# Kernel optimization log

Measured on AMD Instinct MI355X. Metric: run time of the kernel, lower is better.

The kernel has to match this reference:

```python
import jax, jax.numpy as jnp
import numpy as np

N_NODES = 50000
W_IN = 256
W_OUT = 256
HEADS = 8
D_HEAD = W_OUT // HEADS
NUM_EDGE = 3
N_EDGES = 800000
NEG_SLOPE = 0.2


def setup_inputs() -> dict:
    key = jax.random.key(0)
    ks = jax.random.split(key, 10)
    x = jax.random.normal(ks[0], (N_NODES, W_IN), dtype=jnp.float32)
    adj = jax.random.randint(ks[1], (NUM_EDGE, 2, N_EDGES), 0, N_NODES, dtype=jnp.int64)
    sw = 1.0 / np.sqrt(W_IN)
    # Per-edge-type GATConv params, stacked on leading edge-type axis
    Ws = jax.random.normal(ks[2], (NUM_EDGE, W_IN, HEADS * D_HEAD), dtype=jnp.float32) * sw
    a_l = jax.random.normal(ks[3], (NUM_EDGE, HEADS, D_HEAD), dtype=jnp.float32) * 0.1
    a_r = jax.random.normal(ks[4], (NUM_EDGE, HEADS, D_HEAD), dtype=jnp.float32) * 0.1
    bias = jnp.zeros((NUM_EDGE, HEADS * D_HEAD), dtype=jnp.float32)
    # Semantic attention layer: Linear(w_out -> 1)
    att_w = jax.random.normal(ks[5], (W_OUT, 1), dtype=jnp.float32) * (1.0 / np.sqrt(W_OUT))
    att_b = jnp.zeros((1,), dtype=jnp.float32)
    return {"x": x, "adj": adj, "Ws": Ws, "a_l": a_l, "a_r": a_r,
            "bias": bias, "att_w": att_w, "att_b": att_b}


def _gat(x, edge_index, W, al, ar, b):
    # x: [N, W_IN]; edge_index: [2, E]; W: [W_IN, H*D]; al/ar: [H, D]; b: [H*D]
    N = x.shape[0]
    h = (x @ W).reshape(N, HEADS, D_HEAD)            # [N, H, D]
    src, dst = edge_index[0], edge_index[1]
    el = jnp.einsum('nhd,hd->nh', h, al)             # src-side scores [N, H]
    er = jnp.einsum('nhd,hd->nh', h, ar)             # dst-side scores [N, H]
    e = jax.nn.leaky_relu(el[src] + er[dst], NEG_SLOPE)   # [E, H]
    # segment softmax over incoming edges of each dst node
    m = jax.ops.segment_max(e, dst, num_segments=N)       # [N, H]
    e = jnp.exp(e - m[dst])
    s = jax.ops.segment_sum(e, dst, num_segments=N)       # [N, H]
    alpha = e / (s[dst] + 1e-9)                           # [E, H]
    out = jax.ops.segment_sum(alpha[:, :, None] * h[src], dst, num_segments=N)
    return out.reshape(N, HEADS * D_HEAD) + b             # concat heads [N, W_OUT]


def reference(x, adj, Ws, a_l, a_r, bias, att_w, att_b):
    outs = [_gat(x, adj[i], Ws[i], a_l[i], a_r[i], bias[i]) for i in range(NUM_EDGE)]
    stacked = jnp.stack(outs, axis=1)                     # [N, T, W_OUT]
    # AttentionLayer: scores = Linear(stacked) viewed as [N, 1, T]; NO softmax (faithful)
    att = (stacked @ att_w + att_b).reshape(-1, 1, NUM_EDGE)  # [N, 1, T]
    return jnp.matmul(att, stacked).squeeze(1)            # [N, W_OUT]
```

## Files before the change

### kernel.cpp

```cpp
#include <hip/hip_runtime.h>

#define N_NODES 50000
#define W_IN    256
#define W_OUT   256
#define HEADS   8
#define NUM_T   3
#define N_EDGES 800000
#define NEG_SLOPE 0.2f

#define NB      128
#define BSH     9
#define BNODES  512
#define P1_EPT  16
#define P1_CHUNK (256 * P1_EPT)
#define P1_BLOCKS ((N_EDGES + P1_CHUNK - 1) / P1_CHUNK)
#define NB_USED ((N_NODES + BNODES - 1) / BNODES)

typedef __attribute__((ext_vector_type(8))) short bf16x8;
typedef __attribute__((ext_vector_type(4))) float f32x4;

__device__ __forceinline__ unsigned short f2b(float f) {
    unsigned u = __float_as_uint(f);
    u = (u + 0x7fffu + ((u >> 16) & 1u)) >> 16;
    return (unsigned short)u;
}
__device__ __forceinline__ float blo(unsigned u) { return __uint_as_float(u << 16); }
__device__ __forceinline__ float bhi(unsigned u) { return __uint_as_float(u & 0xffff0000u); }

__global__ __launch_bounds__(256) void convert_x(const float* __restrict__ x,
                                                 unsigned short* __restrict__ xb) {
    const size_t i = ((size_t)blockIdx.x * 256 + threadIdx.x) * 4;
    const float4 v = *(const float4*)(x + i);
    ushort4 o;
    o.x = f2b(v.x); o.y = f2b(v.y); o.z = f2b(v.z); o.w = f2b(v.w);
    *(ushort4*)(xb + i) = o;
}

__global__ __launch_bounds__(256) void convert_W(const float* __restrict__ Wsrc,
                                                 unsigned short* __restrict__ Wt) {
    const int t = blockIdx.y;
    const int gid = blockIdx.x * 256 + threadIdx.x;
    const int k = gid >> 8, n = gid & 255;
    Wt[(size_t)t * 65536 + (size_t)n * 256 + k] = f2b(Wsrc[(size_t)t * 65536 + gid]);
}

__global__ __launch_bounds__(256) void p1_hist(const int* __restrict__ adj,
                                               int* __restrict__ bucket_cnt) {
    __shared__ int lh[NB];
    const int t = blockIdx.y;
    const int tid = threadIdx.x;
    if (tid < NB) lh[tid] = 0;
    __syncthreads();

    const int* dstp = adj + (size_t)t * 2 * N_EDGES + N_EDGES;
    const int e0 = blockIdx.x * P1_CHUNK + tid * P1_EPT;
#pragma unroll
    for (int i = 0; i < P1_EPT; ++i) {
        const int e = e0 + i;
        if (e < N_EDGES) atomicAdd(&lh[dstp[e] >> BSH], 1);
    }
    __syncthreads();
    if (tid < NB && lh[tid] > 0) atomicAdd(&bucket_cnt[t * NB + tid], lh[tid]);
}

__global__ __launch_bounds__(128) void p1_scan(const int* __restrict__ bucket_cnt,
                                               int* __restrict__ bucket_ptr,
                                               int* __restrict__ bucket_cur) {
    __shared__ int s[NB];
    const int tid = threadIdx.x;
    for (int t = 0; t < NUM_T; ++t) {
        const int v = bucket_cnt[t * NB + tid];
        s[tid] = v;
        __syncthreads();
        for (int off = 1; off < NB; off <<= 1) {
            int o = (tid >= off) ? s[tid - off] : 0;
            __syncthreads();
            s[tid] += o;
            __syncthreads();
        }
        const int incl = s[tid];
        const int excl = incl - v;
        bucket_ptr[t * (NB + 1) + tid] = excl;
        bucket_cur[t * NB + tid] = excl;
        if (tid == NB - 1) bucket_ptr[t * (NB + 1) + NB] = incl;
        __syncthreads();
    }
}

__global__ __launch_bounds__(256) void p1_scatter(const int* __restrict__ adj,
                                                  int* __restrict__ bucket_cur,
                                                  uint2* __restrict__ part) {
    __shared__ int lh[NB];
    __shared__ int loff[NB];
    __shared__ int lbase[NB];
    __shared__ uint2 buf[P1_CHUNK];
    const int t = blockIdx.y;
    const int tid = threadIdx.x;
    const int lane = tid & 63;
    const int wave = tid >> 6;
    if (tid < NB) lh[tid] = 0;
    __syncthreads();

    const int* srcp = adj + (size_t)t * 2 * N_EDGES;
    const int* dstp = srcp + N_EDGES;
    const int e0 = blockIdx.x * P1_CHUNK + tid * P1_EPT;

    int es[P1_EPT], ed[P1_EPT], rk[P1_EPT];
#pragma unroll
    for (int i = 0; i < P1_EPT; ++i) {
        const int e = e0 + i;
        if (e < N_EDGES) {
            es[i] = srcp[e];
            ed[i] = dstp[e];
            rk[i] = atomicAdd(&lh[ed[i] >> BSH], 1);
        } else {
            ed[i] = -1;
        }
    }
    __syncthreads();

    if (tid < NB && lh[tid] > 0)
        lbase[tid] = atomicAdd(&bucket_cur[t * NB + tid], lh[tid]);
    if (wave == 0) {
        const int c0 = lh[lane * 2], c1 = lh[lane * 2 + 1];
        const int s = c0 + c1;
        int run = s;
        for (int off = 1; off < 64; off <<= 1) {
            const int o = __shfl_up(run, off);
            if (lane >= off) run += o;
        }
        const int base = run - s;
        loff[lane * 2] = base;
        loff[lane * 2 + 1] = base + c0;
    }
    __syncthreads();

#pragma unroll
    for (int i = 0; i < P1_EPT; ++i)
        if (ed[i] >= 0)
            buf[loff[ed[i] >> BSH] + rk[i]] =
                make_uint2((unsigned)es[i], (unsigned)ed[i]);
    __syncthreads();

    uint2* pt = part + (size_t)t * N_EDGES;
    int nvalid = N_EDGES - blockIdx.x * P1_CHUNK;
    if (nvalid > P1_CHUNK) nvalid = P1_CHUNK;
    for (int idx = tid; idx < nvalid; idx += 256) {
        const uint2 e = buf[idx];
        const int b = (int)(e.y >> BSH);
        pt[lbase[b] + (idx - loff[b])] = e;
    }
}

__global__ __launch_bounds__(256) void p2_csr(const uint2* __restrict__ part,
                                              const int* __restrict__ bucket_ptr,
                                              int* __restrict__ row_ptr_all,
                                              int* __restrict__ csr_all) {
    __shared__ int sc[BNODES];
    const int b = blockIdx.x;
    const int t = blockIdx.y;
    const int tid = threadIdx.x;
    const int lane = tid & 63;
    const int wave = tid >> 6;

    const uint2* pt = part + (size_t)t * N_EDGES;
    int* row_ptr = row_ptr_all + (size_t)t * (N_NODES + 1);
    int* csr = csr_all + (size_t)t * N_EDGES;

    const int bp0 = bucket_ptr[t * (NB + 1) + b];
    const int bp1 = bucket_ptr[t * (NB + 1) + b + 1];
    const int node0 = b * BNODES;
    int nn = N_NODES - node0; if (nn > BNODES) nn = BNODES;

    sc[tid] = 0; sc[tid + 256] = 0;
    __syncthreads();

    for (int idx = bp0 + tid; idx < bp1; idx += 256)
        atomicAdd(&sc[pt[idx].y - node0], 1);
    __syncthreads();

    if (wave == 0) {
        int v[8], ex[8];
        int s = 0;
#pragma unroll
        for (int i = 0; i < 8; ++i) { v[i] = sc[lane * 8 + i]; ex[i] = s; s += v[i]; }
        int run = s;
        for (int off = 1; off < 64; off <<= 1) {
            int o = __shfl_up(run, off);
            if (lane >= off) run += o;
        }
        const int base = run - s;
#pragma unroll
        for (int i = 0; i < 8; ++i) sc[lane * 8 + i] = base + ex[i];
    }
    __syncthreads();

    for (int i = tid; i < nn; i += 256) row_ptr[node0 + i] = bp0 + sc[i];
    if (b == NB_USED - 1 && tid == 0) row_ptr[N_NODES] = N_EDGES;
    __syncthreads();

    for (int idx = bp0 + tid; idx < bp1; idx += 256) {
        const uint2 e = pt[idx];
        const int pos = bp0 + atomicAdd(&sc[e.y - node0], 1);
        csr[pos] = (int)e.x;
    }
}

__global__ __launch_bounds__(256) void gemm_fused(const unsigned short* __restrict__ xb,
                                                  const unsigned short* __restrict__ Wt,
                                                  const float* __restrict__ al,
                                                  const float* __restrict__ ar,
                                                  unsigned short* __restrict__ H,
                                                  float* __restrict__ el,
                                                  float* __restrict__ er) {
    __shared__ unsigned short As[64 * 40];
    __shared__ unsigned short Bs[256 * 40];
    __shared__ float els[64 * 8];
    __shared__ float ers[64 * 8];

    const int tid = threadIdx.x;
    const int wave = tid >> 6;
    const int lane = tid & 63;
    const int quad = lane >> 4;
    const int l16 = lane & 15;
    const int m0 = blockIdx.x * 64;

    f32x4 acc[4][4] = {};

    const int arow = tid >> 2;
    const int achunk = (tid & 3) * 8;
    int gm = m0 + arow;
    if (gm > N_NODES - 1) gm = N_NODES - 1;
    const unsigned short* aptr = xb + (size_t)gm * W_IN + achunk;

    for (int k0 = 0; k0 < W_IN; k0 += 32) {
        const uint4 av = *(const uint4*)(aptr + k0);
        *(uint4*)&As[arow * 40 + achunk] = av;
#pragma unroll
        for (int i = 0; i < 4; ++i) {
            const int idx = i * 256 + tid;
            const int brow = idx >> 2;
            const int bch = (idx & 3) * 8;
            const uint4 bv = *(const uint4*)(Wt + (size_t)brow * W_IN + k0 + bch);
            *(uint4*)&Bs[brow * 40 + bch] = bv;
        }
        __syncthreads();

        bf16x8 af[4], bfr[4];
#pragma unroll
        for (int mi = 0; mi < 4; ++mi)
            af[mi] = *(const bf16x8*)&As[(mi * 16 + l16) * 40 + quad * 8];
#pragma unroll
        for (int ni = 0; ni < 4; ++ni)
            bfr[ni] = *(const bf16x8*)&Bs[(wave * 64 + ni * 16 + l16) * 40 + quad * 8];
#pragma unroll
        for (int mi = 0; mi < 4; ++mi)
#pragma unroll
            for (int ni = 0; ni < 4; ++ni)
                acc[mi][ni] = __builtin_amdgcn_mfma_f32_16x16x32_bf16(
                    af[mi], bfr[ni], acc[mi][ni], 0, 0, 0);
        __syncthreads();
    }

#pragma unroll
    for (int mi = 0; mi < 4; ++mi)
#pragma unroll
        for (int reg = 0; reg < 4; ++reg) {
            const int gr = m0 + mi * 16 + quad * 4 + reg;
            if (gr < N_NODES)
#pragma unroll
                for (int ni = 0; ni < 4; ++ni)
                    H[(size_t)gr * W_OUT + wave * 64 + ni * 16 + l16] =
                        f2b(acc[mi][ni][reg]);
        }

    float al4[4], ar4[4];
#pragma unroll
    for (int ni = 0; ni < 4; ++ni) {
        const int c = wave * 64 + ni * 16 + l16;
        al4[ni] = al[c];
        ar4[ni] = ar[c];
    }
#pragma unroll
    for (int mi = 0; mi < 4; ++mi) {
        float pl[4][2] = {}, pr[4][2] = {};
#pragma unroll
        for (int ni = 0; ni < 4; ++ni) {
            const int hl = ni >> 1;
#pragma unroll
            for (int reg = 0; reg < 4; ++reg) {
                pl[reg][hl] += acc[mi][ni][reg] * al4[ni];
                pr[reg][hl] += acc[mi][ni][reg] * ar4[ni];
            }
        }
#pragma unroll
        for (int off = 1; off < 16; off <<= 1)
#pragma unroll
            for (int reg = 0; reg < 4; ++reg)
#pragma unroll
                for (int hl = 0; hl < 2; ++hl) {
                    pl[reg][hl] += __shfl_xor(pl[reg][hl], off);
                    pr[reg][hl] += __shfl_xor(pr[reg][hl], off);
                }
        if (l16 == 0)
#pragma unroll
            for (int reg = 0; reg < 4; ++reg)
#pragma unroll
                for (int hl = 0; hl < 2; ++hl) {
                    const int row = mi * 16 + quad * 4 + reg;
                    els[row * 8 + wave * 2 + hl] = pl[reg][hl];
                    ers[row * 8 + wave * 2 + hl] = pr[reg][hl];
                }
    }
    __syncthreads();

    int nn = N_NODES - m0; if (nn > 64) nn = 64;
    const int nn8 = nn * 8;
    const int i = tid * 4;
    if (i < nn8) {
        *(float4*)(el + (size_t)m0 * 8 + i) = *(float4*)&els[i];
        *(float4*)(er + (size_t)m0 * 8 + i) = *(float4*)&ers[i];
    }
}

__global__ __launch_bounds__(256) void gat_gather(const int* __restrict__ csr_src,
                                                  const int* __restrict__ row_ptr,
                                                  const float* __restrict__ el,
                                                  const float* __restrict__ er,
                                                  const unsigned short* __restrict__ H,
                                                  unsigned short* __restrict__ ot) {
    const int node = (blockIdx.x * blockDim.x + threadIdx.x) >> 6;
    const int lane = threadIdx.x & 63;
    if (node >= N_NODES) return;
    const int half = lane >> 5;
    const int d8 = lane & 31;
    const int hh = d8 >> 2;

    const int beg = row_ptr[node];
    const int deg = row_ptr[node + 1] - beg;
    const float erv = er[(size_t)node * HEADS + hh];

    float2 acc[4] = {};
    float ssum = 0.f;

    if (deg > 0) {
        int mysrc = (lane < deg) ? csr_src[beg + lane] : 0;
        const int npairs = (deg + 1) >> 1;

        int src0 = __shfl(mysrc, half);
        uint4 u0 = *(const uint4*)(H + (size_t)src0 * W_OUT + d8 * 8);
        float elv0 = el[(size_t)src0 * HEADS + hh];

        for (int q = 0; q < npairs; ++q) {
            int src1 = 0; uint4 u1 = u0; float elv1 = 0.f;
            const int q1 = q + 1;
            if (q1 < npairs) {
                if ((q1 & 31) == 0) {
                    const int cb = beg + (q1 >> 5) * 64;
                    mysrc = (cb + lane < beg + deg) ? csr_src[cb + lane] : 0;
                }
                src1 = __shfl(mysrc, (2 * q1 + half) & 63);
                u1 = *(const uint4*)(H + (size_t)src1 * W_OUT + d8 * 8);
                elv1 = el[(size_t)src1 * HEADS + hh];
            }
            float v = elv0 + erv;
            v = (v > 0.f) ? v : NEG_SLOPE * v;
            const float w = (2 * q + half < deg) ? __expf(v) : 0.f;
            acc[0].x += w * blo(u0.x); acc[0].y += w * bhi(u0.x);
            acc[1].x += w * blo(u0.y); acc[1].y += w * bhi(u0.y);
            acc[2].x += w * blo(u0.z); acc[2].y += w * bhi(u0.z);
            acc[3].x += w * blo(u0.w); acc[3].y += w * bhi(u0.w);
            ssum += w;
            src0 = src1; u0 = u1; elv0 = elv1;
        }
    }

#pragma unroll
    for (int i = 0; i < 4; ++i) {
        acc[i].x += __shfl_xor(acc[i].x, 32);
        acc[i].y += __shfl_xor(acc[i].y, 32);
    }
    ssum += __shfl_xor(ssum, 32);

    if (half == 0) {
        const float inv = 1.f / (ssum + 1e-9f);
        unsigned short o8[8];
#pragma unroll
        for (int i = 0; i < 4; ++i) {
            o8[2 * i]     = f2b(acc[i].x * inv);
            o8[2 * i + 1] = f2b(acc[i].y * inv);
        }
        *(uint4*)(ot + (size_t)node * W_OUT + d8 * 8) = *(const uint4*)o8;
    }
}

__global__ __launch_bounds__(256) void combine(const unsigned short* __restrict__ ot0,
                                               const unsigned short* __restrict__ ot1,
                                               const unsigned short* __restrict__ ot2,
                                               const float* __restrict__ bias,
                                               const float* __restrict__ att_w,
                                               const float* __restrict__ att_b,
                                               float* __restrict__ out) {
    const int gw = (blockIdx.x * blockDim.x + threadIdx.x) >> 6;
    const int lane = threadIdx.x & 63;
    if (gw >= N_NODES) return;

    const float4 aw = *(const float4*)(att_w + lane * 4);
    const size_t base = (size_t)gw * W_OUT + lane * 4;

    float4 v[NUM_T];
    float p[NUM_T];
    const unsigned short* ots[NUM_T] = {ot0, ot1, ot2};
#pragma unroll
    for (int t = 0; t < NUM_T; ++t) {
        const uint2 u = *(const uint2*)(ots[t] + base);
        const float4 bv = *(const float4*)(bias + t * W_OUT + lane * 4);
        float4 hv;
        hv.x = blo(u.x) + bv.x;
        hv.y = bhi(u.x) + bv.y;
        hv.z = blo(u.y) + bv.z;
        hv.w = bhi(u.y) + bv.w;
        v[t] = hv;
        p[t] = hv.x * aw.x + hv.y * aw.y + hv.z * aw.z + hv.w * aw.w;
    }
#pragma unroll
    for (int off = 1; off < 64; off <<= 1) {
        p[0] += __shfl_xor(p[0], off);
        p[1] += __shfl_xor(p[1], off);
        p[2] += __shfl_xor(p[2], off);
    }
    const float ab = att_b[0];
    const float a0 = p[0] + ab, a1 = p[1] + ab, a2 = p[2] + ab;
    float4 o;
    o.x = a0 * v[0].x + a1 * v[1].x + a2 * v[2].x;
    o.y = a0 * v[0].y + a1 * v[1].y + a2 * v[2].y;
    o.z = a0 * v[0].z + a1 * v[1].z + a2 * v[2].z;
    o.w = a0 * v[0].w + a1 * v[1].w + a2 * v[2].w;
    *(float4*)(out + base) = o;
}

extern "C" void kernel_launch(void* const* d_in, const int* in_sizes, int n_in,
                              void* d_out, int out_size, void* d_ws, size_t ws_size,
                              hipStream_t stream) {
    const float* x     = (const float*)d_in[0];
    const int*   adj   = (const int*)d_in[1];
    const float* Ws    = (const float*)d_in[2];
    const float* a_l   = (const float*)d_in[3];
    const float* a_r   = (const float*)d_in[4];
    const float* bias  = (const float*)d_in[5];
    const float* att_w = (const float*)d_in[6];
    const float* att_b = (const float*)d_in[7];
    float* out = (float*)d_out;

    char* w = (char*)d_ws;
    unsigned short* xb = (unsigned short*)w; w += (size_t)N_NODES * W_IN * 2;
    unsigned short* H  = (unsigned short*)w; w += (size_t)N_NODES * W_OUT * 2;
    unsigned short* Wt = (unsigned short*)w; w += (size_t)NUM_T * 65536 * 2;
    unsigned short* ot0 = (unsigned short*)w; w += (size_t)N_NODES * W_OUT * 2;
    unsigned short* ot1 = (unsigned short*)w; w += (size_t)N_NODES * W_OUT * 2;
    unsigned short* ot2 = (unsigned short*)w; w += (size_t)N_NODES * W_OUT * 2;
    float* el  = (float*)w; w += (size_t)N_NODES * HEADS * 4;
    float* er  = (float*)w; w += (size_t)N_NODES * HEADS * 4;
    int* csr_src = (int*)w; w += (size_t)NUM_T * N_EDGES * 4;
    int* row_ptr = (int*)w; w += (size_t)NUM_T * (N_NODES + 1) * 4;
    int* bucket_cnt = (int*)w; w += NUM_T * NB * 4;
    int* bucket_ptr = (int*)w; w += NUM_T * (NB + 1) * 4;
    int* bucket_cur = (int*)w; w += NUM_T * NB * 4;
    uint2* part = (uint2*)ot0;

    unsigned short* ot[NUM_T] = {ot0, ot1, ot2};
    const int node_wave_blocks = (N_NODES + 3) / 4;
    const int gemm_blocks = (N_NODES + 63) / 64;

    hipMemsetAsync(bucket_cnt, 0, NUM_T * NB * sizeof(int), stream);
    convert_x<<<12500, 256, 0, stream>>>(x, xb);
    convert_W<<<dim3(256, NUM_T), 256, 0, stream>>>(Ws, Wt);
    p1_hist<<<dim3(P1_BLOCKS, NUM_T), 256, 0, stream>>>(adj, bucket_cnt);
    p1_scan<<<1, 128, 0, stream>>>(bucket_cnt, bucket_ptr, bucket_cur);
    p1_scatter<<<dim3(P1_BLOCKS, NUM_T), 256, 0, stream>>>(adj, bucket_cur, part);
    p2_csr<<<dim3(NB_USED, NUM_T), 256, 0, stream>>>(part, bucket_ptr, row_ptr,
                                                     csr_src);

    for (int t = 0; t < NUM_T; ++t) {
        gemm_fused<<<gemm_blocks, 256, 0, stream>>>(
            xb, Wt + (size_t)t * 65536, a_l + t * 256, a_r + t * 256, H, el, er);
        gat_gather<<<node_wave_blocks, 256, 0, stream>>>(
            csr_src + (size_t)t * N_EDGES, row_ptr + (size_t)t * (N_NODES + 1),
            el, er, H, ot[t]);
    }

    combine<<<node_wave_blocks, 256, 0, stream>>>(ot0, ot1, ot2, bias, att_w,
                                                  att_b, out);
}
```

Baseline: 499.7 us.

## Process four edges per wave step in GAT gather with deeper prefetch

```diff
diff --git a/kernel.cpp b/kernel.cpp
--- a/kernel.cpp
+++ b/kernel.cpp
@@ -332,65 +332,113 @@
     const int node = (blockIdx.x * blockDim.x + threadIdx.x) >> 6;
     const int lane = threadIdx.x & 63;
     if (node >= N_NODES) return;
-    const int half = lane >> 5;
-    const int d8 = lane & 31;
-    const int hh = d8 >> 2;
+    const int g   = lane >> 4;
+    const int d16 = lane & 15;
+    const int h0  = d16 >> 2;
 
     const int beg = row_ptr[node];
     const int deg = row_ptr[node + 1] - beg;
-    const float erv = er[(size_t)node * HEADS + hh];
-
-    float2 acc[4] = {};
-    float ssum = 0.f;
+
+    const float er_lo = er[(size_t)node * HEADS + h0];
+    const float er_hi = er[(size_t)node * HEADS + h0 + 4];
+
+    float2 alo[4] = {}, ahi[4] = {};
+    float ssl = 0.f, ssh = 0.f;
 
     if (deg > 0) {
         int mysrc = (lane < deg) ? csr_src[beg + lane] : 0;
-        const int npairs = (deg + 1) >> 1;
-
-        int src0 = __shfl(mysrc, half);
-        uint4 u0 = *(const uint4*)(H + (size_t)src0 * W_OUT + d8 * 8);
-        float elv0 = el[(size_t)src0 * HEADS + hh];
-
-        for (int q = 0; q < npairs; ++q) {
-            int src1 = 0; uint4 u1 = u0; float elv1 = 0.f;
-            const int q1 = q + 1;
-            if (q1 < npairs) {
-                if ((q1 & 31) == 0) {
-                    const int cb = beg + (q1 >> 5) * 64;
-                    mysrc = (cb + lane < beg + deg) ? csr_src[cb + lane] : 0;
-                }
-                src1 = __shfl(mysrc, (2 * q1 + half) & 63);
-                u1 = *(const uint4*)(H + (size_t)src1 * W_OUT + d8 * 8);
-                elv1 = el[(size_t)src1 * HEADS + hh];
+        const int nq = (deg + 3) >> 2;
+
+        uint4 AL = {}, AH = {}, BL = {}, BH = {};
+        uint4 nAL = {}, nAH = {}, nBL = {}, nBH = {};
+        float Ae0 = 0.f, Ae1 = 0.f, Be0 = 0.f, Be1 = 0.f;
+        float nAe0 = 0.f, nAe1 = 0.f, nBe0 = 0.f, nBe1 = 0.f;
+
+#define REFRESH(qp)                                                           \
+        do {                                                                  \
+            if ((((qp) & 15) == 0) && ((qp) > 0)) {                           \
+                const int base = beg + ((qp) >> 4) * 64;                      \
+                mysrc = (base + lane < beg + deg) ? csr_src[base + lane] : 0; \
+            }                                                                 \
+        } while (0)
+
+#define PFQ(qp, UL, UH, E0, E1)                                               \
+        do {                                                                  \
+            const int e = 4 * (qp) + g;                                       \
+            const int s = __shfl(mysrc, e & 63);                              \
+            const unsigned short* hp = H + (size_t)s * W_OUT + d16 * 8;       \
+            UL = *(const uint4*)hp;                                           \
+            UH = *(const uint4*)(hp + 128);                                   \
+            E0 = el[(size_t)s * HEADS + h0];                                  \
+            E1 = el[(size_t)s * HEADS + h0 + 4];                              \
+        } while (0)
+
+#define CQ(qp, UL, UH, E0, E1)                                                \
+        do {                                                                  \
+            const bool val = (4 * (qp) + g) < deg;                            \
+            float vl = E0 + er_lo; vl = fmaxf(vl, NEG_SLOPE * vl);            \
+            float vh = E1 + er_hi; vh = fmaxf(vh, NEG_SLOPE * vh);            \
+            const float wl = val ? __expf(vl) : 0.f;                          \
+            const float wh = val ? __expf(vh) : 0.f;                          \
+            ssl += wl; ssh += wh;                                             \
+            alo[0].x += wl * blo(UL.x); alo[0].y += wl * bhi(UL.x);           \
+            alo[1].x += wl * blo(UL.y); alo[1].y += wl * bhi(UL.y);           \
+            alo[2].x += wl * blo(UL.z); alo[2].y += wl * bhi(UL.z);           \
+            alo[3].x += wl * blo(UL.w); alo[3].y += wl * bhi(UL.w);           \
+            ahi[0].x += wh * blo(UH.x); ahi[0].y += wh * bhi(UH.x);           \
+            ahi[1].x += wh * blo(UH.y); ahi[1].y += wh * bhi(UH.y);           \
+            ahi[2].x += wh * blo(UH.z); ahi[2].y += wh * bhi(UH.z);           \
+            ahi[3].x += wh * blo(UH.w); ahi[3].y += wh * bhi(UH.w);           \
+        } while (0)
+
+        PFQ(0, AL, AH, Ae0, Ae1);
+        PFQ(1, BL, BH, Be0, Be1);
+
+        const int nm = (nq + 1) >> 1;
+        for (int m = 0; m < nm; ++m) {
+            const int q2 = 2 * m + 2;
+            const bool more = q2 < nq;
+            if (more) {
+                REFRESH(q2);
+                PFQ(q2,     nAL, nAH, nAe0, nAe1);
+                PFQ(q2 + 1, nBL, nBH, nBe0, nBe1);
             }
-            float v = elv0 + erv;
-            v = (v > 0.f) ? v : NEG_SLOPE * v;
-            const float w = (2 * q + half < deg) ? __expf(v) : 0.f;
-            acc[0].x += w * blo(u0.x); acc[0].y += w * bhi(u0.x);
-            acc[1].x += w * blo(u0.y); acc[1].y += w * bhi(u0.y);
-            acc[2].x += w * blo(u0.z); acc[2].y += w * bhi(u0.z);
-            acc[3].x += w * blo(u0.w); acc[3].y += w * bhi(u0.w);
-            ssum += w;
-            src0 = src1; u0 = u1; elv0 = elv1;
-        }
+            CQ(2 * m,     AL, AH, Ae0, Ae1);
+            CQ(2 * m + 1, BL, BH, Be0, Be1);
+            if (more) {
+                AL = nAL; AH = nAH; Ae0 = nAe0; Ae1 = nAe1;
+                BL = nBL; BH = nBH; Be0 = nBe0; Be1 = nBe1;
+            }
+        }
+#undef REFRESH
+#undef PFQ
+#undef CQ
     }
 
 #pragma unroll
     for (int i = 0; i < 4; ++i) {
-        acc[i].x += __shfl_xor(acc[i].x, 32);
-        acc[i].y += __shfl_xor(acc[i].y, 32);
-    }
-    ssum += __shfl_xor(ssum, 32);
-
-    if (half == 0) {
-        const float inv = 1.f / (ssum + 1e-9f);
-        unsigned short o8[8];
-#pragma unroll
-        for (int i = 0; i < 4; ++i) {
-            o8[2 * i]     = f2b(acc[i].x * inv);
-            o8[2 * i + 1] = f2b(acc[i].y * inv);
-        }
-        *(uint4*)(ot + (size_t)node * W_OUT + d8 * 8) = *(const uint4*)o8;
+        alo[i].x += __shfl_xor(alo[i].x, 16); alo[i].x += __shfl_xor(alo[i].x, 32);
+        alo[i].y += __shfl_xor(alo[i].y, 16); alo[i].y += __shfl_xor(alo[i].y, 32);
+        ahi[i].x += __shfl_xor(ahi[i].x, 16); ahi[i].x += __shfl_xor(ahi[i].x, 32);
+        ahi[i].y += __shfl_xor(ahi[i].y, 16); ahi[i].y += __shfl_xor(ahi[i].y, 32);
+    }
+    ssl += __shfl_xor(ssl, 16); ssl += __shfl_xor(ssl, 32);
+    ssh += __shfl_xor(ssh, 16); ssh += __shfl_xor(ssh, 32);
+
+    if (lane < 16) {
+        const float il = 1.f / (ssl + 1e-9f);
+        const float ih = 1.f / (ssh + 1e-9f);
+        unsigned short o[8];
+        o[0] = f2b(alo[0].x * il); o[1] = f2b(alo[0].y * il);
+        o[2] = f2b(alo[1].x * il); o[3] = f2b(alo[1].y * il);
+        o[4] = f2b(alo[2].x * il); o[5] = f2b(alo[2].y * il);
+        o[6] = f2b(alo[3].x * il); o[7] = f2b(alo[3].y * il);
+        *(uint4*)(ot + (size_t)node * W_OUT + d16 * 8) = *(const uint4*)o;
+        o[0] = f2b(ahi[0].x * ih); o[1] = f2b(ahi[0].y * ih);
+        o[2] = f2b(ahi[1].x * ih); o[3] = f2b(ahi[1].y * ih);
+        o[4] = f2b(ahi[2].x * ih); o[5] = f2b(ahi[2].y * ih);
+        o[6] = f2b(ahi[3].x * ih); o[7] = f2b(ahi[3].y * ih);
+        *(uint4*)(ot + (size_t)node * W_OUT + 128 + d16 * 8) = *(const uint4*)o;
     }
 }
 
```

Result: no change. 505.0 us (+1.1%).

## Overlap next edge-type GEMM with current gather in interleaved fused launch

Applied to the files above, without the earlier changes.

```diff
diff --git a/kernel.cpp b/kernel.cpp
--- a/kernel.cpp
+++ b/kernel.cpp
@@ -15,6 +15,12 @@
 #define P1_CHUNK (256 * P1_EPT)
 #define P1_BLOCKS ((N_EDGES + P1_CHUNK - 1) / P1_CHUNK)
 #define NB_USED ((N_NODES + BNODES - 1) / BNODES)
+
+#define GEMM_BLOCKS ((N_NODES + 63) / 64)
+#define GATHER_BLOCKS ((N_NODES + 3) / 4)
+#define FUSE_STRIDE 17
+#define FUSED_BLOCKS (GEMM_BLOCKS + GATHER_BLOCKS)
+#define GEMM_SMEM 29696
 
 typedef __attribute__((ext_vector_type(8))) short bf16x8;
 typedef __attribute__((ext_vector_type(4))) float f32x4;
@@ -206,24 +212,25 @@
     }
 }
 
-__global__ __launch_bounds__(256) void gemm_fused(const unsigned short* __restrict__ xb,
-                                                  const unsigned short* __restrict__ Wt,
-                                                  const float* __restrict__ al,
-                                                  const float* __restrict__ ar,
-                                                  unsigned short* __restrict__ H,
-                                                  float* __restrict__ el,
-                                                  float* __restrict__ er) {
-    __shared__ unsigned short As[64 * 40];
-    __shared__ unsigned short Bs[256 * 40];
-    __shared__ float els[64 * 8];
-    __shared__ float ers[64 * 8];
-
-    const int tid = threadIdx.x;
+__device__ __forceinline__ void gemm_body(const int bm, const int tid,
+                                          unsigned char* smem,
+                                          const unsigned short* __restrict__ xb,
+                                          const unsigned short* __restrict__ Wt,
+                                          const float* __restrict__ al,
+                                          const float* __restrict__ ar,
+                                          unsigned short* __restrict__ H,
+                                          float* __restrict__ el,
+                                          float* __restrict__ er) {
+    unsigned short* As = (unsigned short*)smem;
+    unsigned short* Bs = (unsigned short*)(smem + 5120);
+    float* els = (float*)(smem + 25600);
+    float* ers = (float*)(smem + 27648);
+
     const int wave = tid >> 6;
     const int lane = tid & 63;
     const int quad = lane >> 4;
     const int l16 = lane & 15;
-    const int m0 = blockIdx.x * 64;
+    const int m0 = bm * 64;
 
     f32x4 acc[4][4] = {};
 
@@ -323,15 +330,13 @@
     }
 }
 
-__global__ __launch_bounds__(256) void gat_gather(const int* __restrict__ csr_src,
-                                                  const int* __restrict__ row_ptr,
-                                                  const float* __restrict__ el,
-                                                  const float* __restrict__ er,
-                                                  const unsigned short* __restrict__ H,
-                                                  unsigned short* __restrict__ ot) {
-    const int node = (blockIdx.x * blockDim.x + threadIdx.x) >> 6;
-    const int lane = threadIdx.x & 63;
-    if (node >= N_NODES) return;
+__device__ __forceinline__ void gather_body(const int node, const int lane,
+                                            const int* __restrict__ csr_src,
+                                            const int* __restrict__ row_ptr,
+                                            const float* __restrict__ el,
+                                            const float* __restrict__ er,
+                                            const unsigned short* __restrict__ H,
+                                            unsigned short* __restrict__ ot) {
     const int half = lane >> 5;
     const int d8 = lane & 31;
     const int hh = d8 >> 2;
@@ -394,6 +399,50 @@
     }
 }
 
+__global__ __launch_bounds__(256) void gemm_fused(const unsigned short* __restrict__ xb,
+                                                  const unsigned short* __restrict__ Wt,
+                                                  const float* __restrict__ al,
+                                                  const float* __restrict__ ar,
+                                                  unsigned short* __restrict__ H,
+                                                  float* __restrict__ el,
+                                                  float* __restrict__ er) {
+    __shared__ __attribute__((aligned(16))) unsigned char smem[GEMM_SMEM];
+    gemm_body(blockIdx.x, threadIdx.x, smem, xb, Wt, al, ar, H, el, er);
+}
+
+__global__ __launch_bounds__(256) void gat_gather(const int* __restrict__ csr_src,
+                                                  const int* __restrict__ row_ptr,
+                                                  const float* __restrict__ el,
+                                                  const float* __restrict__ er,
+                                                  const unsigned short* __restrict__ H,
+                                                  unsigned short* __restrict__ ot) {
+    const int node = (blockIdx.x * blockDim.x + threadIdx.x) >> 6;
+    if (node >= N_NODES) return;
+    gather_body(node, threadIdx.x & 63, csr_src, row_ptr, el, er, H, ot);
+}
+
+__global__ __launch_bounds__(256) void fused_gg(
+    const unsigned short* __restrict__ xb, const unsigned short* __restrict__ Wt,
+    const float* __restrict__ al, const float* __restrict__ ar,
+    unsigned short* __restrict__ Hout, float* __restrict__ el_out,
+    float* __restrict__ er_out,
+    const int* __restrict__ csr_src, const int* __restrict__ row_ptr,
+    const float* __restrict__ el_in, const float* __restrict__ er_in,
+    const unsigned short* __restrict__ Hin, unsigned short* __restrict__ ot) {
+    __shared__ __attribute__((aligned(16))) unsigned char smem[GEMM_SMEM];
+    const int p = blockIdx.x;
+    const int q = p / FUSE_STRIDE;
+    if (p % FUSE_STRIDE == 0) {
+        gemm_body(q, threadIdx.x, smem, xb, Wt, al, ar, Hout, el_out, er_out);
+    } else {
+        const int gb = p - q - 1;
+        const int node = gb * 4 + (threadIdx.x >> 6);
+        if (node < N_NODES)
+            gather_body(node, threadIdx.x & 63, csr_src, row_ptr, el_in, er_in,
+                        Hin, ot);
+    }
+}
+
 __global__ __launch_bounds__(256) void combine(const unsigned short* __restrict__ ot0,
                                                const unsigned short* __restrict__ ot1,
                                                const unsigned short* __restrict__ ot2,
@@ -454,23 +503,22 @@
 
     char* w = (char*)d_ws;
     unsigned short* xb = (unsigned short*)w; w += (size_t)N_NODES * W_IN * 2;
-    unsigned short* H  = (unsigned short*)w; w += (size_t)N_NODES * W_OUT * 2;
+    unsigned short* H0 = (unsigned short*)w; w += (size_t)N_NODES * W_OUT * 2;
     unsigned short* Wt = (unsigned short*)w; w += (size_t)NUM_T * 65536 * 2;
     unsigned short* ot0 = (unsigned short*)w; w += (size_t)N_NODES * W_OUT * 2;
     unsigned short* ot1 = (unsigned short*)w; w += (size_t)N_NODES * W_OUT * 2;
     unsigned short* ot2 = (unsigned short*)w; w += (size_t)N_NODES * W_OUT * 2;
-    float* el  = (float*)w; w += (size_t)N_NODES * HEADS * 4;
-    float* er  = (float*)w; w += (size_t)N_NODES * HEADS * 4;
+    float* el0 = (float*)w; w += (size_t)N_NODES * HEADS * 4;
+    float* er0 = (float*)w; w += (size_t)N_NODES * HEADS * 4;
+    float* el1 = (float*)w; w += (size_t)N_NODES * HEADS * 4;
+    float* er1 = (float*)w; w += (size_t)N_NODES * HEADS * 4;
     int* csr_src = (int*)w; w += (size_t)NUM_T * N_EDGES * 4;
     int* row_ptr = (int*)w; w += (size_t)NUM_T * (N_NODES + 1) * 4;
     int* bucket_cnt = (int*)w; w += NUM_T * NB * 4;
     int* bucket_ptr = (int*)w; w += NUM_T * (NB + 1) * 4;
     int* bucket_cur = (int*)w; w += NUM_T * NB * 4;
     uint2* part = (uint2*)ot0;
-
-    unsigned short* ot[NUM_T] = {ot0, ot1, ot2};
-    const int node_wave_blocks = (N_NODES + 3) / 4;
-    const int gemm_blocks = (N_NODES + 63) / 64;
+    unsigned short* H1 = ot2;
 
     hipMemsetAsync(bucket_cnt, 0, NUM_T * NB * sizeof(int), stream);
     convert_x<<<12500, 256, 0, stream>>>(x, xb);
@@ -481,14 +529,18 @@
     p2_csr<<<dim3(NB_USED, NUM_T), 256, 0, stream>>>(part, bucket_ptr, row_ptr,
                                                      csr_src);
 
-    for (int t = 0; t < NUM_T; ++t) {
-        gemm_fused<<<gemm_blocks, 256, 0, stream>>>(
-            xb, Wt + (size_t)t * 65536, a_l + t * 256, a_r + t * 256, H, el, er);
-        gat_gather<<<node_wave_blocks, 256, 0, stream>>>(
-            csr_src + (size_t)t * N_EDGES, row_ptr + (size_t)t * (N_NODES + 1),
-            el, er, H, ot[t]);
-    }
-
-    combine<<<node_wave_blocks, 256, 0, stream>>>(ot0, ot1, ot2, bias, att_w,
-                                                  att_b, out);
-}
+    gemm_fused<<<GEMM_BLOCKS, 256, 0, stream>>>(
+        xb, Wt, a_l, a_r, H0, el0, er0);
+    fused_gg<<<FUSED_BLOCKS, 256, 0, stream>>>(
+        xb, Wt + 65536, a_l + 256, a_r + 256, H1, el1, er1,
+        csr_src, row_ptr, el0, er0, H0, ot0);
+    fused_gg<<<FUSED_BLOCKS, 256, 0, stream>>>(
+        xb, Wt + 2 * 65536, a_l + 512, a_r + 512, H0, el0, er0,
+        csr_src + N_EDGES, row_ptr + (N_NODES + 1), el1, er1, H1, ot1);
+    gat_gather<<<GATHER_BLOCKS, 256, 0, stream>>>(
+        csr_src + 2 * (size_t)N_EDGES, row_ptr + 2 * (N_NODES + 1),
+        el0, er0, H0, ot2);
+
+    combine<<<GATHER_BLOCKS, 256, 0, stream>>>(ot0, ot1, ot2, bias, att_w,
+                                               att_b, out);
+}
```

Result: slower. 650.2 us (+30.1%).
